# Performance work log

Measured on AMD Instinct MI355X. Metric: run time of the kernel, lower is better.

The kernel has to match this reference:

```python
import jax, jax.numpy as jnp
import numpy as np

B, L, D, T = 2, 2048, 1536, 2
INITRANGE = 0.1

def setup_inputs() -> dict:
    key = jax.random.key(0)
    k1, k2 = jax.random.split(key)
    hidden_states = jax.random.normal(k1, (B, L, D), dtype=jnp.float32)
    # decoder: Linear(2*D, T) with uniform(-0.1, 0.1) weight, zero bias
    W = jax.random.uniform(k2, (T, 2 * D), dtype=jnp.float32, minval=-INITRANGE, maxval=INITRANGE)
    b = jnp.zeros((T,), dtype=jnp.float32)
    return {"hidden_states": hidden_states, "W": W, "b": b}

def reference(hidden_states, W, b):
    # Faithful fused version of:
    #   prod = h[:,:,None,:] * h[:,None,:,:]; diff = h[:,:,None,:] - h[:,None,:,:]
    #   logits = cat(prod, diff, -1) @ W.T + b
    # Split W into the product half and the difference half.
    d = hidden_states.shape[-1]
    Wp, Wd = W[:, :d], W[:, d:]                      # [T, D] each
    # prod term: sum_d h[b,i,d] * h[b,j,d] * Wp[t,d]
    hw = jnp.einsum('bid,td->btid', hidden_states, Wp)          # [B,T,L,D]
    prod_logits = jnp.einsum('btid,bjd->bijt', hw, hidden_states)  # [B,L,L,T]
    # diff term: (h[b,i]-h[b,j]) @ Wd.T = (h@Wd.T)[b,i] - (h@Wd.T)[b,j]
    hd = jnp.einsum('bid,td->bit', hidden_states, Wd)           # [B,L,T]
    diff_logits = hd[:, :, None, :] - hd[:, None, :, :]         # [B,L,L,T]
    logits = prod_logits + diff_logits + b
    # symmetrize over the (i, j) pair axes
    logits = (logits + jnp.transpose(logits, (0, 2, 1, 3))) * 0.5
    return logits
```

## Files before the change

kernel.cpp:

```cpp
#include <hip/hip_runtime.h>
#include <hip/hip_bf16.h>
#include <stdint.h>

#define B_ 2
#define L_ 2048
#define D_ 1536

typedef __attribute__((ext_vector_type(4))) float  f32x4;
typedef __attribute__((ext_vector_type(8))) __bf16 bf16x8;

__device__ __forceinline__ unsigned short f2bf(float f) {
  unsigned int u = __float_as_uint(f);
  u += 0x7fffu + ((u >> 16) & 1u);
  return (unsigned short)(u >> 16);
}

__global__ __launch_bounds__(256) void conv_kernel(
    const float* __restrict__ hs, const float* __restrict__ W,
    unsigned short* __restrict__ X, unsigned short* __restrict__ P) {
  const int idx  = blockIdx.x * 256 + threadIdx.x;
  const int base = idx * 4;
  const int d    = base % D_;
  const float4 h  = *(const float4*)(hs + base);
  const float4 w0 = *(const float4*)(W + d);
  const float4 w1 = *(const float4*)(W + 2 * D_ + d);
  ushort4 x, p0, p1;
  x.x  = f2bf(h.x);        x.y  = f2bf(h.y);        x.z  = f2bf(h.z);        x.w  = f2bf(h.w);
  p0.x = f2bf(h.x * w0.x); p0.y = f2bf(h.y * w0.y); p0.z = f2bf(h.z * w0.z); p0.w = f2bf(h.w * w0.w);
  p1.x = f2bf(h.x * w1.x); p1.y = f2bf(h.y * w1.y); p1.z = f2bf(h.z * w1.z); p1.w = f2bf(h.w * w1.w);
  *(ushort4*)(X + base) = x;
  *(ushort4*)(P + base) = p0;
  *(ushort4*)(P + (size_t)B_ * L_ * D_ + base) = p1;
}

__global__ __launch_bounds__(256, 2) void gemm_kernel(
    const unsigned short* __restrict__ X, const unsigned short* __restrict__ P,
    const float* __restrict__ bias, float2* __restrict__ out) {
  __shared__ unsigned short As0[2 * 128 * 32];
  __shared__ unsigned short As1[2 * 128 * 32];
  __shared__ unsigned short Bs [2 * 128 * 32];

  const int tid = threadIdx.x;

  const int id     = blockIdx.x;
  const int xcd    = id & 7;
  const int u      = id >> 3;
  const int within = u & 15;
  const int pp     = u >> 4;
  const int Pp     = pp * 8 + xcd;
  const int bz     = Pp >> 4;
  const int pr     = Pp & 15;
  const int I0     = ((pr >> 2) * 4 + (within >> 2)) * 128;
  const int J0     = ((pr & 3)  * 4 + (within & 3))  * 128;

  const int srow = tid >> 2;
  const int cs   = tid & 3;
  const int gc   = cs ^ ((srow >> 1) & 3);
  const int scol = gc * 8;
  const int ldst = tid * 8;

  const size_t planeB = (size_t)B_ * L_ * D_;
  const unsigned short* pA0 = P + ((size_t)(bz * L_ + I0 + srow)) * D_ + scol;
  const unsigned short* pA1 = pA0 + planeB;
  const unsigned short* pB  = X + ((size_t)(bz * L_ + J0 + srow)) * D_ + scol;

  const int lane = tid & 63;
  const int w    = tid >> 6;
  const int wi   = (w & 1) * 64;
  const int wj   = (w >> 1) * 64;
  const int lr   = lane & 15;
  const int q    = lane >> 4;
  const int ccol = (q ^ ((lr >> 1) & 3)) * 8;

  int aoff[4], boff[4];
#pragma unroll
  for (int m = 0; m < 4; ++m) {
    aoff[m] = (wi + m * 16 + lr) * 32 + ccol;
    boff[m] = (wj + m * 16 + lr) * 32 + ccol;
  }

  f32x4 acc0[4][4] = {};
  f32x4 acc1[4][4] = {};

  uint4 ra0l, ra0h, ra1l, ra1h, rbl, rbh;
  uint4 sa0l, sa0h, sa1l, sa1h, sbl, sbh;

#define GLOAD0(koff)                                      \
  do {                                                    \
    ra0l = *(const uint4*)(pA0 + (koff));                 \
    ra0h = *(const uint4*)(pA0 + (koff) + 64 * D_);       \
    ra1l = *(const uint4*)(pA1 + (koff));                 \
    ra1h = *(const uint4*)(pA1 + (koff) + 64 * D_);       \
    rbl  = *(const uint4*)(pB  + (koff));                 \
    rbh  = *(const uint4*)(pB  + (koff) + 64 * D_);       \
  } while (0)
#define GLOAD1(koff)                                      \
  do {                                                    \
    sa0l = *(const uint4*)(pA0 + (koff));                 \
    sa0h = *(const uint4*)(pA0 + (koff) + 64 * D_);       \
    sa1l = *(const uint4*)(pA1 + (koff));                 \
    sa1h = *(const uint4*)(pA1 + (koff) + 64 * D_);       \
    sbl  = *(const uint4*)(pB  + (koff));                 \
    sbh  = *(const uint4*)(pB  + (koff) + 64 * D_);       \
  } while (0)
#define DSW(buf, A0L, A0H, A1L, A1H, BL, BH)              \
  do {                                                    \
    *(uint4*)(As0 + (buf) * 4096 + ldst)        = A0L;    \
    *(uint4*)(As0 + (buf) * 4096 + ldst + 2048) = A0H;    \
    *(uint4*)(As1 + (buf) * 4096 + ldst)        = A1L;    \
    *(uint4*)(As1 + (buf) * 4096 + ldst + 2048) = A1H;    \
    *(uint4*)(Bs  + (buf) * 4096 + ldst)        = BL;     \
    *(uint4*)(Bs  + (buf) * 4096 + ldst + 2048) = BH;     \
  } while (0)
#define COMPUTE(buf)                                                           \
  do {                                                                         \
    const unsigned short* A0b = As0 + (buf) * 4096;                            \
    const unsigned short* A1b = As1 + (buf) * 4096;                            \
    const unsigned short* Bb  = Bs  + (buf) * 4096;                            \
    bf16x8 a0f[4], a1f[4], bf_[4];                                             \
    _Pragma("unroll") for (int m = 0; m < 4; ++m) {                            \
      a0f[m] = *(const bf16x8*)(A0b + aoff[m]);                                \
      a1f[m] = *(const bf16x8*)(A1b + aoff[m]);                                \
    }                                                                          \
    _Pragma("unroll") for (int n = 0; n < 4; ++n)                              \
      bf_[n] = *(const bf16x8*)(Bb + boff[n]);                                 \
    _Pragma("unroll") for (int m = 0; m < 4; ++m)                              \
      _Pragma("unroll") for (int n = 0; n < 4; ++n) {                          \
        acc0[m][n] = __builtin_amdgcn_mfma_f32_16x16x32_bf16(a0f[m], bf_[n],   \
                                                             acc0[m][n], 0, 0, 0); \
        acc1[m][n] = __builtin_amdgcn_mfma_f32_16x16x32_bf16(a1f[m], bf_[n],   \
                                                             acc1[m][n], 0, 0, 0); \
      }                                                                        \
  } while (0)

  GLOAD0(0);
  for (int k = 0; k < D_ / 32; k += 2) {
    DSW(0, ra0l, ra0h, ra1l, ra1h, rbl, rbh);
    GLOAD1((k + 1) * 32);
    __syncthreads();
    COMPUTE(0);
    DSW(1, sa0l, sa0h, sa1l, sa1h, sbl, sbh);
    if (k + 2 < D_ / 32) GLOAD0((k + 2) * 32);
    __syncthreads();
    COMPUTE(1);
  }
#undef GLOAD0
#undef GLOAD1
#undef DSW
#undef COMPUTE

  const float bias0 = bias[0], bias1 = bias[1];
#pragma unroll
  for (int m = 0; m < 4; ++m) {
#pragma unroll
    for (int r = 0; r < 4; ++r) {
      const int i = I0 + wi + m * 16 + q * 4 + r;
      float2* orow = out + (size_t)(bz * L_ + i) * L_ + (J0 + wj + lr);
#pragma unroll
      for (int n = 0; n < 4; ++n) {
        float2 v;
        v.x = acc0[m][n][r] + bias0;
        v.y = acc1[m][n][r] + bias1;
        orow[n * 16] = v;
      }
    }
  }
}

extern "C" void kernel_launch(void* const* d_in, const int* in_sizes, int n_in,
                              void* d_out, int out_size, void* d_ws, size_t ws_size,
                              hipStream_t stream) {
  const float* hs   = (const float*)d_in[0];
  const float* W    = (const float*)d_in[1];
  const float* bias = (const float*)d_in[2];

  unsigned short* X = (unsigned short*)d_ws;
  unsigned short* P = X + (size_t)B_ * L_ * D_;

  const int nconv = (B_ * L_ * D_ / 4) / 256;
  conv_kernel<<<nconv, 256, 0, stream>>>(hs, W, X, P);

  gemm_kernel<<<512, 256, 0, stream>>>(X, P, bias, (float2*)d_out);
}
```

Baseline: 144.4 us.

## Restructure GEMM with direct global-to-LDS loads, larger tiles, and phased pipeline

Rewrites the bf16 MFMA GEMM to use 512-thread blocks over 128x256 output tiles with a BK of 64. Operands are copied straight from global memory into LDS with global_load_lds, and the LDS layout uses an XOR swizzle. The K loop is split into four sub-phases with explicit vmcnt/lgkmcnt waits, barriers and s_setprio, so loads of the next stage overlap with MFMA work on the current one. The aim is to cut register staging and the exposed load latency and to raise operand reuse, at the cost of 128KB of LDS per block, more barriers, and fragile hand-tuned wait counts.

```diff
diff --git a/kernel.cpp b/kernel.cpp
--- a/kernel.cpp
+++ b/kernel.cpp
@@ -5,6 +5,7 @@
 #define B_ 2
 #define L_ 2048
 #define D_ 1536
+#define NT (D_ / 64)
 
 typedef __attribute__((ext_vector_type(4))) float  f32x4;
 typedef __attribute__((ext_vector_type(8))) __bf16 bf16x8;
@@ -33,135 +34,179 @@
   *(ushort4*)(P + (size_t)B_ * L_ * D_ + base) = p1;
 }
 
-__global__ __launch_bounds__(256, 2) void gemm_kernel(
+__device__ __forceinline__ void gload16(const unsigned short* g, unsigned short* l) {
+  __builtin_amdgcn_global_load_lds(
+      (const __attribute__((address_space(1))) unsigned int*)g,
+      (__attribute__((address_space(3))) unsigned int*)l, 16, 0, 0);
+}
+
+#define A0OFF 0
+#define A1OFF 8192
+#define B0OFF 16384
+#define B1OFF 24576
+
+__global__ __launch_bounds__(512, 2) void gemm_kernel(
     const unsigned short* __restrict__ X, const unsigned short* __restrict__ P,
     const float* __restrict__ bias, float2* __restrict__ out) {
-  __shared__ unsigned short As0[2 * 128 * 32];
-  __shared__ unsigned short As1[2 * 128 * 32];
-  __shared__ unsigned short Bs [2 * 128 * 32];
+  __shared__ unsigned short lds[65536];
 
   const int tid = threadIdx.x;
 
-  const int id     = blockIdx.x;
-  const int xcd    = id & 7;
-  const int u      = id >> 3;
-  const int within = u & 15;
-  const int pp     = u >> 4;
-  const int Pp     = pp * 8 + xcd;
-  const int bz     = Pp >> 4;
-  const int pr     = Pp & 15;
-  const int I0     = ((pr >> 2) * 4 + (within >> 2)) * 128;
-  const int J0     = ((pr & 3)  * 4 + (within & 3))  * 128;
-
-  const int srow = tid >> 2;
-  const int cs   = tid & 3;
-  const int gc   = cs ^ ((srow >> 1) & 3);
-  const int scol = gc * 8;
-  const int ldst = tid * 8;
+  const int id  = blockIdx.x;
+  const int swz = (id & 7) * 32 + (id >> 3);
+  const int bz  = swz >> 7;
+  const int t2  = swz & 127;
+  const int I0  = (t2 >> 3) * 128;
+  const int J0  = (t2 & 7) * 256;
 
   const size_t planeB = (size_t)B_ * L_ * D_;
-  const unsigned short* pA0 = P + ((size_t)(bz * L_ + I0 + srow)) * D_ + scol;
-  const unsigned short* pA1 = pA0 + planeB;
-  const unsigned short* pB  = X + ((size_t)(bz * L_ + J0 + srow)) * D_ + scol;
+  const unsigned short* gA0 = P + (size_t)(bz * L_ + I0) * D_;
+  const unsigned short* gA1 = gA0 + planeB;
+  const unsigned short* gB0 = X + (size_t)(bz * L_ + J0) * D_;
+  const unsigned short* gB1 = gB0 + (size_t)128 * D_;
+
+  const int    sr    = tid >> 3;
+  const int    sc    = (tid & 7) ^ (sr & 7);
+  const size_t lgoff = (size_t)sr * D_ + (size_t)(sc * 8);
+  const int    wuni  = (tid >> 6) * 512;
 
   const int lane = tid & 63;
   const int w    = tid >> 6;
-  const int wi   = (w & 1) * 64;
-  const int wj   = (w >> 1) * 64;
+  const int wr   = w & 1;
+  const int wc   = w >> 1;
   const int lr   = lane & 15;
   const int q    = lane >> 4;
-  const int ccol = (q ^ ((lr >> 1) & 3)) * 8;
-
-  int aoff[4], boff[4];
+  const int swd  = lr & 7;
+  const int csw0 = ((0 + q) ^ swd) * 8;
+  const int csw1 = ((4 + q) ^ swd) * 8;
+  int aRow[4], bRow[2];
+#pragma unroll
+  for (int m = 0; m < 4; ++m) aRow[m] = (wr * 64 + m * 16 + lr) * 64;
+#pragma unroll
+  for (int n = 0; n < 2; ++n) bRow[n] = (wc * 32 + n * 16 + lr) * 64;
+
+  f32x4  acc[8][4] = {};
+  bf16x8 aF[4][2], bF[2][2];
+
+#define STG(REG, GBASE, KTN)                                                  \
+  do {                                                                        \
+    const unsigned short* g0 = (GBASE) + lgoff + (size_t)((KTN) * 64);        \
+    gload16(g0,                 lds + (REG) + wuni);                          \
+    gload16(g0 + (size_t)64 * D_, lds + (REG) + 4096 + wuni);                 \
+  } while (0)
+
+#define RDA(CB, MH)                                                           \
+  do {                                                                        \
+    _Pragma("unroll") for (int m = 0; m < 4; ++m) {                           \
+      aF[m][0] = *(const bf16x8*)(lds + (CB) + (MH) * 8192 + aRow[m] + csw0); \
+      aF[m][1] = *(const bf16x8*)(lds + (CB) + (MH) * 8192 + aRow[m] + csw1); \
+    }                                                                         \
+  } while (0)
+
+#define RDB(CB, NH)                                                           \
+  do {                                                                        \
+    _Pragma("unroll") for (int n = 0; n < 2; ++n) {                           \
+      bF[n][0] = *(const bf16x8*)(lds + (CB) + 16384 + (NH) * 8192 + bRow[n] + csw0); \
+      bF[n][1] = *(const bf16x8*)(lds + (CB) + 16384 + (NH) * 8192 + bRow[n] + csw1); \
+    }                                                                         \
+  } while (0)
+
+#define MM(MH, NH)                                                            \
+  do {                                                                        \
+    _Pragma("unroll") for (int kk = 0; kk < 2; ++kk)                          \
+    _Pragma("unroll") for (int m = 0; m < 4; ++m)                             \
+    _Pragma("unroll") for (int n = 0; n < 2; ++n)                             \
+      acc[(MH) * 4 + m][(NH) * 2 + n] = __builtin_amdgcn_mfma_f32_16x16x32_bf16( \
+          aF[m][kk], bF[n][kk], acc[(MH) * 4 + m][(NH) * 2 + n], 0, 0, 0);    \
+  } while (0)
+
+#define BAR()   __builtin_amdgcn_s_barrier()
+#define LGKM0() asm volatile("s_waitcnt lgkmcnt(0)" ::: "memory")
+#define WVM(n)  asm volatile("s_waitcnt vmcnt(" #n ")" ::: "memory")
+#define PRIO1() __builtin_amdgcn_s_setprio(1)
+#define PRIO0() __builtin_amdgcn_s_setprio(0)
+
+#define KSTEP(CB, NB, KTN)                                                    \
+  do {                                                                        \
+                                                                      \
+    RDA(CB, 0); RDB(CB, 0);                                                   \
+    STG((NB) + A0OFF, gA0, KTN); STG((NB) + B0OFF, gB0, KTN);                 \
+    BAR(); LGKM0();                                                           \
+    PRIO1(); MM(0, 0); PRIO0();                                               \
+    WVM(6); BAR();                                                            \
+                                                                      \
+    RDB(CB, 1);                                                               \
+    STG((NB) + B1OFF, gB1, KTN);                                              \
+    BAR(); LGKM0();                                                           \
+    PRIO1(); MM(0, 1); PRIO0();                                               \
+    WVM(6); BAR();                                                            \
+                                                                      \
+    RDA(CB, 1);                                                               \
+    STG((NB) + A1OFF, gA1, KTN);                                              \
+    BAR(); LGKM0();                                                           \
+    PRIO1(); MM(1, 1); PRIO0();                                               \
+    BAR();                                                                    \
+                                        \
+    RDB(CB, 0);                                                               \
+    BAR(); LGKM0();                                                           \
+    PRIO1(); MM(1, 0); PRIO0();                                               \
+    WVM(4); BAR();                                                            \
+  } while (0)
+
+#define KTAIL(CB)                                                             \
+  do {                                                                        \
+    RDA(CB, 0); RDB(CB, 0);                                                   \
+    BAR(); LGKM0();                                                           \
+    PRIO1(); MM(0, 0); PRIO0();                                               \
+    WVM(2); BAR();                                                            \
+    RDB(CB, 1);                                                               \
+    BAR(); LGKM0();                                                           \
+    PRIO1(); MM(0, 1); PRIO0();                                               \
+    WVM(0); BAR();                                                            \
+    RDA(CB, 1);                                                               \
+    BAR(); LGKM0();                                                           \
+    PRIO1(); MM(1, 1); PRIO0();                                               \
+    BAR();                                                                    \
+    RDB(CB, 0);                                                               \
+    LGKM0();                                                                  \
+    PRIO1(); MM(1, 0); PRIO0();                                               \
+  } while (0)
+
+  STG(A0OFF, gA0, 0); STG(B0OFF, gB0, 0);
+  STG(B1OFF, gB1, 0);
+  STG(A1OFF, gA1, 0);
+  WVM(4); BAR();
+
+#pragma unroll 1
+  for (int it = 0; it < 11; ++it) {
+    const int kt0 = 2 * it;
+    KSTEP(0,     32768, kt0 + 1);
+    KSTEP(32768, 0,     kt0 + 2);
+  }
+  KSTEP(0, 32768, 23);
+  KTAIL(32768);
+
+#undef KSTEP
+#undef KTAIL
+#undef STG
+#undef RDA
+#undef RDB
+#undef MM
+
+  const float bias0 = bias[0], bias1 = bias[1];
 #pragma unroll
   for (int m = 0; m < 4; ++m) {
-    aoff[m] = (wi + m * 16 + lr) * 32 + ccol;
-    boff[m] = (wj + m * 16 + lr) * 32 + ccol;
-  }
-
-  f32x4 acc0[4][4] = {};
-  f32x4 acc1[4][4] = {};
-
-  uint4 ra0l, ra0h, ra1l, ra1h, rbl, rbh;
-  uint4 sa0l, sa0h, sa1l, sa1h, sbl, sbh;
-
-#define GLOAD0(koff)                                      \
-  do {                                                    \
-    ra0l = *(const uint4*)(pA0 + (koff));                 \
-    ra0h = *(const uint4*)(pA0 + (koff) + 64 * D_);       \
-    ra1l = *(const uint4*)(pA1 + (koff));                 \
-    ra1h = *(const uint4*)(pA1 + (koff) + 64 * D_);       \
-    rbl  = *(const uint4*)(pB  + (koff));                 \
-    rbh  = *(const uint4*)(pB  + (koff) + 64 * D_);       \
-  } while (0)
-#define GLOAD1(koff)                                      \
-  do {                                                    \
-    sa0l = *(const uint4*)(pA0 + (koff));                 \
-    sa0h = *(const uint4*)(pA0 + (koff) + 64 * D_);       \
-    sa1l = *(const uint4*)(pA1 + (koff));                 \
-    sa1h = *(const uint4*)(pA1 + (koff) + 64 * D_);       \
-    sbl  = *(const uint4*)(pB  + (koff));                 \
-    sbh  = *(const uint4*)(pB  + (koff) + 64 * D_);       \
-  } while (0)
-#define DSW(buf, A0L, A0H, A1L, A1H, BL, BH)              \
-  do {                                                    \
-    *(uint4*)(As0 + (buf) * 4096 + ldst)        = A0L;    \
-    *(uint4*)(As0 + (buf) * 4096 + ldst + 2048) = A0H;    \
-    *(uint4*)(As1 + (buf) * 4096 + ldst)        = A1L;    \
-    *(uint4*)(As1 + (buf) * 4096 + ldst + 2048) = A1H;    \
-    *(uint4*)(Bs  + (buf) * 4096 + ldst)        = BL;     \
-    *(uint4*)(Bs  + (buf) * 4096 + ldst + 2048) = BH;     \
-  } while (0)
-#define COMPUTE(buf)                                                           \
-  do {                                                                         \
-    const unsigned short* A0b = As0 + (buf) * 4096;                            \
-    const unsigned short* A1b = As1 + (buf) * 4096;                            \
-    const unsigned short* Bb  = Bs  + (buf) * 4096;                            \
-    bf16x8 a0f[4], a1f[4], bf_[4];                                             \
-    _Pragma("unroll") for (int m = 0; m < 4; ++m) {                            \
-      a0f[m] = *(const bf16x8*)(A0b + aoff[m]);                                \
-      a1f[m] = *(const bf16x8*)(A1b + aoff[m]);                                \
-    }                                                                          \
-    _Pragma("unroll") for (int n = 0; n < 4; ++n)                              \
-      bf_[n] = *(const bf16x8*)(Bb + boff[n]);                                 \
-    _Pragma("unroll") for (int m = 0; m < 4; ++m)                              \
-      _Pragma("unroll") for (int n = 0; n < 4; ++n) {                          \
-        acc0[m][n] = __builtin_amdgcn_mfma_f32_16x16x32_bf16(a0f[m], bf_[n],   \
-                                                             acc0[m][n], 0, 0, 0); \
-        acc1[m][n] = __builtin_amdgcn_mfma_f32_16x16x32_bf16(a1f[m], bf_[n],   \
-                                                             acc1[m][n], 0, 0, 0); \
-      }                                                                        \
-  } while (0)
-
-  GLOAD0(0);
-  for (int k = 0; k < D_ / 32; k += 2) {
-    DSW(0, ra0l, ra0h, ra1l, ra1h, rbl, rbh);
-    GLOAD1((k + 1) * 32);
-    __syncthreads();
-    COMPUTE(0);
-    DSW(1, sa0l, sa0h, sa1l, sa1h, sbl, sbh);
-    if (k + 2 < D_ / 32) GLOAD0((k + 2) * 32);
-    __syncthreads();
-    COMPUTE(1);
-  }
-#undef GLOAD0
-#undef GLOAD1
-#undef DSW
-#undef COMPUTE
-
-  const float bias0 = bias[0], bias1 = bias[1];
-#pragma unroll
-  for (int m = 0; m < 4; ++m) {
 #pragma unroll
     for (int r = 0; r < 4; ++r) {
-      const int i = I0 + wi + m * 16 + q * 4 + r;
-      float2* orow = out + (size_t)(bz * L_ + i) * L_ + (J0 + wj + lr);
+      const int i = I0 + wr * 64 + m * 16 + q * 4 + r;
+      float2* orow = out + (size_t)(bz * L_ + i) * L_;
 #pragma unroll
       for (int n = 0; n < 4; ++n) {
+        const int j = J0 + (n >> 1) * 128 + wc * 32 + (n & 1) * 16 + lr;
         float2 v;
-        v.x = acc0[m][n][r] + bias0;
-        v.y = acc1[m][n][r] + bias1;
-        orow[n * 16] = v;
+        v.x = acc[m][n][r] + bias0;
+        v.y = acc[m + 4][n][r] + bias1;
+        orow[j] = v;
       }
     }
   }
@@ -180,5 +225,5 @@
   const int nconv = (B_ * L_ * D_ / 4) / 256;
   conv_kernel<<<nconv, 256, 0, stream>>>(hs, W, X, P);
 
-  gemm_kernel<<<512, 256, 0, stream>>>(X, P, bias, (float2*)d_out);
-}
+  gemm_kernel<<<256, 512, 0, stream>>>(X, P, bias, (float2*)d_out);
+}
```

After: 134.6 us. -6.8%, faster.

## Use direct global-to-LDS loads with larger 256-wide tiles and 8x8 wave accumulators

Applied to the files above, without the earlier changes.

Rewrites the GEMM main loop to use global_load_lds, which copies data straight from global memory into LDS and removes the register staging and LDS store step. The per-block tile grows to 128 rows times two weight planes by 256 columns, with K steps of 64 and double-buffered 128KB LDS. Each wave now holds an 8x8 accumulator array. The grid halves to 256 blocks with one block per CU, which trades occupancy and latency hiding for more data reuse and a larger register footprint.

```diff
diff --git a/kernel.cpp b/kernel.cpp
--- a/kernel.cpp
+++ b/kernel.cpp
@@ -33,120 +33,99 @@
   *(ushort4*)(P + (size_t)B_ * L_ * D_ + base) = p1;
 }
 
-__global__ __launch_bounds__(256, 2) void gemm_kernel(
+__device__ __forceinline__ void gload16(const unsigned short* g, unsigned short* l) {
+  __builtin_amdgcn_global_load_lds(
+      (const __attribute__((address_space(1))) unsigned int*)g,
+      (__attribute__((address_space(3))) unsigned int*)l, 16, 0, 0);
+}
+
+__global__ __launch_bounds__(256, 1) void gemm_kernel(
     const unsigned short* __restrict__ X, const unsigned short* __restrict__ P,
     const float* __restrict__ bias, float2* __restrict__ out) {
-  __shared__ unsigned short As0[2 * 128 * 32];
-  __shared__ unsigned short As1[2 * 128 * 32];
-  __shared__ unsigned short Bs [2 * 128 * 32];
+  __shared__ unsigned short lds[65536];
 
   const int tid = threadIdx.x;
 
-  const int id     = blockIdx.x;
-  const int xcd    = id & 7;
-  const int u      = id >> 3;
-  const int within = u & 15;
-  const int pp     = u >> 4;
-  const int Pp     = pp * 8 + xcd;
-  const int bz     = Pp >> 4;
-  const int pr     = Pp & 15;
-  const int I0     = ((pr >> 2) * 4 + (within >> 2)) * 128;
-  const int J0     = ((pr & 3)  * 4 + (within & 3))  * 128;
-
-  const int srow = tid >> 2;
-  const int cs   = tid & 3;
-  const int gc   = cs ^ ((srow >> 1) & 3);
-  const int scol = gc * 8;
-  const int ldst = tid * 8;
+  const int id  = blockIdx.x;
+  const int swz = (id & 7) * 32 + (id >> 3);
+  const int bz  = swz >> 7;
+  const int t2  = swz & 127;
+  const int I0  = (t2 >> 3) * 128;
+  const int J0  = (t2 & 7) * 256;
 
   const size_t planeB = (size_t)B_ * L_ * D_;
-  const unsigned short* pA0 = P + ((size_t)(bz * L_ + I0 + srow)) * D_ + scol;
-  const unsigned short* pA1 = pA0 + planeB;
-  const unsigned short* pB  = X + ((size_t)(bz * L_ + J0 + srow)) * D_ + scol;
+
+  const int    sr    = tid >> 3;
+  const int    sc    = (tid & 7) ^ (sr & 7);
+  const size_t lgoff = (size_t)sr * D_ + (size_t)(sc * 8);
+  const int    w     = tid >> 6;
+
+  const unsigned short* gA0 = P +          ((size_t)(bz * L_ + I0)) * D_ + lgoff;
+  const unsigned short* gA1 = P + planeB + ((size_t)(bz * L_ + I0)) * D_ + lgoff;
+  const unsigned short* gA2 = P +          ((size_t)(bz * L_ + I0 + 64)) * D_ + lgoff;
+  const unsigned short* gA3 = P + planeB + ((size_t)(bz * L_ + I0 + 64)) * D_ + lgoff;
+  const unsigned short* gB  = X +          ((size_t)(bz * L_ + J0)) * D_ + lgoff;
 
   const int lane = tid & 63;
-  const int w    = tid >> 6;
-  const int wi   = (w & 1) * 64;
-  const int wj   = (w >> 1) * 64;
+  const int wr   = w >> 1;
+  const int wc   = w & 1;
   const int lr   = lane & 15;
   const int q    = lane >> 4;
-  const int ccol = (q ^ ((lr >> 1) & 3)) * 8;
+  const int swd  = lr & 7;
+  const int csw0 = ((0 + q) ^ swd) * 8;
+  const int csw1 = ((4 + q) ^ swd) * 8;
+  const int aBase = (wr * 128 + lr) * 64;
+  const int bBase = 16384 + (wc * 128 + lr) * 64;
 
-  int aoff[4], boff[4];
-#pragma unroll
-  for (int m = 0; m < 4; ++m) {
-    aoff[m] = (wi + m * 16 + lr) * 32 + ccol;
-    boff[m] = (wj + m * 16 + lr) * 32 + ccol;
-  }
+  f32x4 acc[8][8] = {};
 
-  f32x4 acc0[4][4] = {};
-  f32x4 acc1[4][4] = {};
-
-  uint4 ra0l, ra0h, ra1l, ra1h, rbl, rbh;
-  uint4 sa0l, sa0h, sa1l, sa1h, sbl, sbh;
-
-#define GLOAD0(koff)                                      \
-  do {                                                    \
-    ra0l = *(const uint4*)(pA0 + (koff));                 \
-    ra0h = *(const uint4*)(pA0 + (koff) + 64 * D_);       \
-    ra1l = *(const uint4*)(pA1 + (koff));                 \
-    ra1h = *(const uint4*)(pA1 + (koff) + 64 * D_);       \
-    rbl  = *(const uint4*)(pB  + (koff));                 \
-    rbh  = *(const uint4*)(pB  + (koff) + 64 * D_);       \
-  } while (0)
-#define GLOAD1(koff)                                      \
-  do {                                                    \
-    sa0l = *(const uint4*)(pA0 + (koff));                 \
-    sa0h = *(const uint4*)(pA0 + (koff) + 64 * D_);       \
-    sa1l = *(const uint4*)(pA1 + (koff));                 \
-    sa1h = *(const uint4*)(pA1 + (koff) + 64 * D_);       \
-    sbl  = *(const uint4*)(pB  + (koff));                 \
-    sbh  = *(const uint4*)(pB  + (koff) + 64 * D_);       \
-  } while (0)
-#define DSW(buf, A0L, A0H, A1L, A1H, BL, BH)              \
-  do {                                                    \
-    *(uint4*)(As0 + (buf) * 4096 + ldst)        = A0L;    \
-    *(uint4*)(As0 + (buf) * 4096 + ldst + 2048) = A0H;    \
-    *(uint4*)(As1 + (buf) * 4096 + ldst)        = A1L;    \
-    *(uint4*)(As1 + (buf) * 4096 + ldst + 2048) = A1H;    \
-    *(uint4*)(Bs  + (buf) * 4096 + ldst)        = BL;     \
-    *(uint4*)(Bs  + (buf) * 4096 + ldst + 2048) = BH;     \
-  } while (0)
-#define COMPUTE(buf)                                                           \
+#define STG(NB, KT)                                                            \
   do {                                                                         \
-    const unsigned short* A0b = As0 + (buf) * 4096;                            \
-    const unsigned short* A1b = As1 + (buf) * 4096;                            \
-    const unsigned short* Bb  = Bs  + (buf) * 4096;                            \
-    bf16x8 a0f[4], a1f[4], bf_[4];                                             \
-    _Pragma("unroll") for (int m = 0; m < 4; ++m) {                            \
-      a0f[m] = *(const bf16x8*)(A0b + aoff[m]);                                \
-      a1f[m] = *(const bf16x8*)(A1b + aoff[m]);                                \
-    }                                                                          \
-    _Pragma("unroll") for (int n = 0; n < 4; ++n)                              \
-      bf_[n] = *(const bf16x8*)(Bb + boff[n]);                                 \
-    _Pragma("unroll") for (int m = 0; m < 4; ++m)                              \
-      _Pragma("unroll") for (int n = 0; n < 4; ++n) {                          \
-        acc0[m][n] = __builtin_amdgcn_mfma_f32_16x16x32_bf16(a0f[m], bf_[n],   \
-                                                             acc0[m][n], 0, 0, 0); \
-        acc1[m][n] = __builtin_amdgcn_mfma_f32_16x16x32_bf16(a1f[m], bf_[n],   \
-                                                             acc1[m][n], 0, 0, 0); \
-      }                                                                        \
+    const size_t ko = (size_t)(KT) * 64;                                       \
+    gload16(gA0 + ko,                    lds + (NB) + (0 * 64 + 0 * 32 + w * 8) * 64); \
+    gload16(gA0 + ko + (size_t)32 * D_,  lds + (NB) + (0 * 64 + 1 * 32 + w * 8) * 64); \
+    gload16(gA1 + ko,                    lds + (NB) + (1 * 64 + 0 * 32 + w * 8) * 64); \
+    gload16(gA1 + ko + (size_t)32 * D_,  lds + (NB) + (1 * 64 + 1 * 32 + w * 8) * 64); \
+    gload16(gA2 + ko,                    lds + (NB) + (2 * 64 + 0 * 32 + w * 8) * 64); \
+    gload16(gA2 + ko + (size_t)32 * D_,  lds + (NB) + (2 * 64 + 1 * 32 + w * 8) * 64); \
+    gload16(gA3 + ko,                    lds + (NB) + (3 * 64 + 0 * 32 + w * 8) * 64); \
+    gload16(gA3 + ko + (size_t)32 * D_,  lds + (NB) + (3 * 64 + 1 * 32 + w * 8) * 64); \
+    _Pragma("unroll") for (int l = 0; l < 8; ++l)                              \
+      gload16(gB + ko + (size_t)(l * 32) * D_,                                 \
+              lds + (NB) + 16384 + (l * 32 + w * 8) * 64);                     \
   } while (0)
 
-  GLOAD0(0);
-  for (int k = 0; k < D_ / 32; k += 2) {
-    DSW(0, ra0l, ra0h, ra1l, ra1h, rbl, rbh);
-    GLOAD1((k + 1) * 32);
-    __syncthreads();
-    COMPUTE(0);
-    DSW(1, sa0l, sa0h, sa1l, sa1h, sbl, sbh);
-    if (k + 2 < D_ / 32) GLOAD0((k + 2) * 32);
-    __syncthreads();
-    COMPUTE(1);
+#define COMPUTE(CB)                                                            \
+  do {                                                                         \
+    _Pragma("unroll") for (int kk = 0; kk < 2; ++kk) {                         \
+      const int cs = kk ? csw1 : csw0;                                         \
+      bf16x8 aF[8], bF[8];                                                     \
+      _Pragma("unroll") for (int m = 0; m < 8; ++m)                            \
+        aF[m] = *(const bf16x8*)(lds + (CB) + aBase + m * 1024 + cs);          \
+      _Pragma("unroll") for (int n = 0; n < 8; ++n)                            \
+        bF[n] = *(const bf16x8*)(lds + (CB) + bBase + n * 1024 + cs);          \
+      _Pragma("unroll") for (int m = 0; m < 8; ++m)                            \
+        _Pragma("unroll") for (int n = 0; n < 8; ++n)                          \
+          acc[m][n] = __builtin_amdgcn_mfma_f32_16x16x32_bf16(                 \
+              aF[m], bF[n], acc[m][n], 0, 0, 0);                               \
+    }                                                                          \
+  } while (0)
+
+  STG(0, 0);
+  asm volatile("s_waitcnt vmcnt(0)" ::: "memory");
+  __builtin_amdgcn_s_barrier();
+
+#pragma unroll 1
+  for (int kt = 0; kt < 24; ++kt) {
+    const int cb = (kt & 1) * 32768;
+    if (kt < 23) STG(32768 - cb, kt + 1);
+    COMPUTE(cb);
+    if (kt < 23) {
+      asm volatile("s_waitcnt vmcnt(0)" ::: "memory");
+      __builtin_amdgcn_s_barrier();
+    }
   }
-#undef GLOAD0
-#undef GLOAD1
-#undef DSW
+#undef STG
 #undef COMPUTE
 
   const float bias0 = bias[0], bias1 = bias[1];
@@ -154,13 +133,13 @@
   for (int m = 0; m < 4; ++m) {
 #pragma unroll
     for (int r = 0; r < 4; ++r) {
-      const int i = I0 + wi + m * 16 + q * 4 + r;
-      float2* orow = out + (size_t)(bz * L_ + i) * L_ + (J0 + wj + lr);
+      const int i = I0 + wr * 64 + m * 16 + q * 4 + r;
+      float2* orow = out + (size_t)(bz * L_ + i) * L_ + (J0 + wc * 128 + lr);
 #pragma unroll
-      for (int n = 0; n < 4; ++n) {
+      for (int n = 0; n < 8; ++n) {
         float2 v;
-        v.x = acc0[m][n][r] + bias0;
-        v.y = acc1[m][n][r] + bias1;
+        v.x = acc[m][n][r] + bias0;
+        v.y = acc[m + 4][n][r] + bias1;
         orow[n * 16] = v;
       }
     }
@@ -180,5 +159,5 @@
   const int nconv = (B_ * L_ * D_ / 4) / 256;
   conv_kernel<<<nconv, 256, 0, stream>>>(hs, W, X, P);
 
-  gemm_kernel<<<512, 256, 0, stream>>>(X, P, bias, (float2*)d_out);
+  gemm_kernel<<<256, 256, 0, stream>>>(X, P, bias, (float2*)d_out);
 }
```

Result: no change. 144.2 us (-0.1%).
